# Performance work log

Hardware: AMD Instinct MI355X
Metric: run time of the kernel (lower is better)

## Reference

```python
import jax, jax.numpy as jnp
import numpy as np

N_ATOMS = 16384
B_GRAPHS = 64
K_CLUSTERS = 64          # clusters per molecule
M_CLUSTERS = B_GRAPHS * K_CLUSTERS
HID = 256                # hidden_channels (== node_attr feature dim)
FIL = 256                # num_filters
ECH = 64                 # edge_channels (num gaussians)
L_INT = 6                # num_interactions
CUTOFF = 10.0
LN2 = float(np.log(2.0))


def _ssp(x):
    # ShiftedSoftplus
    return jax.nn.softplus(x) - LN2


def setup_inputs() -> dict:
    key = jax.random.key(0)
    ks = jax.random.split(key, 12)
    pos = jax.random.normal(ks[0], (N_ATOMS, 3), jnp.float32) * 2.0
    node_attr = jax.random.normal(ks[1], (N_ATOMS, HID), jnp.float32)
    atoms_per_cluster = N_ATOMS // M_CLUSTERS
    subgraph_index = (jnp.arange(N_ATOMS) // atoms_per_cluster).astype(jnp.int64)
    batch = (jnp.arange(N_ATOMS) // (N_ATOMS // B_GRAPHS)).astype(jnp.int64)
    s = 0.05
    params = {
        "mlp_w1": jax.random.normal(ks[2], (L_INT, ECH, FIL), jnp.float32) * s,
        "mlp_b1": jnp.zeros((L_INT, FIL), jnp.float32),
        "mlp_w2": jax.random.normal(ks[3], (L_INT, FIL, FIL), jnp.float32) * s,
        "mlp_b2": jnp.zeros((L_INT, FIL), jnp.float32),
        "lin1_w": jax.random.normal(ks[4], (L_INT, HID, FIL), jnp.float32) * s,  # no bias
        "lin2_w": jax.random.normal(ks[5], (L_INT, FIL, HID), jnp.float32) * s,
        "lin2_b": jnp.zeros((L_INT, HID), jnp.float32),
        "lin_w":  jax.random.normal(ks[6], (L_INT, HID, HID), jnp.float32) * s,
        "lin_b":  jnp.zeros((L_INT, HID), jnp.float32),
    }
    return {"pos": pos, "node_attr": node_attr,
            "subgraph_index": subgraph_index, "batch": batch,
            "num_graphs": B_GRAPHS, "clusters_per_graph": K_CLUSTERS, **params}


def _complete_graph_edges(num_graphs, clusters_per_graph):
    # static (numpy) construction of per-molecule complete graph, no self loops
    K = clusters_per_graph
    i = np.arange(K)
    pr, pc = np.meshgrid(i, i, indexing='ij')
    m = pr != pc
    pr, pc = pr[m], pc[m]                       # (K*(K-1),)
    off = np.arange(num_graphs)[:, None] * K    # (B,1)
    row = jnp.asarray((off + pr[None, :]).reshape(-1))
    col = jnp.asarray((off + pc[None, :]).reshape(-1))
    return row, col


def reference(pos, node_attr, subgraph_index, batch, num_graphs, clusters_per_graph,
              mlp_w1, mlp_b1, mlp_w2, mlp_b2, lin1_w, lin2_w, lin2_b, lin_w, lin_b):
    M = num_graphs * clusters_per_graph
    # ---- coarse_grain: scatter-mean atoms into clusters ----
    cnt = jax.ops.segment_sum(jnp.ones((pos.shape[0],), pos.dtype), subgraph_index, num_segments=M)
    cnt = jnp.maximum(cnt, 1.0)[:, None]
    cluster_pos = jax.ops.segment_sum(pos, subgraph_index, num_segments=M) / cnt        # (M,3)
    cluster_attr = jax.ops.segment_sum(node_attr, subgraph_index, num_segments=M) / cnt  # (M,H)

    # ---- complete graph per molecule ----
    row, col = _complete_graph_edges(num_graphs, clusters_per_graph)
    edge_length = jnp.linalg.norm(cluster_pos[row] - cluster_pos[col], axis=1)          # (E,)

    # ---- GaussianSmearing ----
    offset = jnp.linspace(0.0, CUTOFF, ECH)
    coeff = -0.5 / (offset[1] - offset[0]) ** 2
    edge_attr = jnp.exp(coeff * (edge_length[:, None] - offset[None, :]) ** 2)          # (E,ECH)

    # smooth cutoff envelope
    C = 0.5 * (jnp.cos(edge_length * jnp.pi / CUTOFF) + 1.0)
    C = C * (edge_length <= CUTOFF).astype(C.dtype)                                     # (E,)

    # ---- SchNetEncoder (embed_node=False) ----
    h = cluster_attr
    for l in range(L_INT):
        # filter-generating MLP
        W = _ssp(edge_attr @ mlp_w1[l] + mlp_b1[l]) @ mlp_w2[l] + mlp_b2[l]             # (E,F)
        W = W * C[:, None]
        x = h @ lin1_w[l]                                                               # (M,F)
        agg = jax.ops.segment_sum(x[row] * W, col, num_segments=M)                      # (M,F)
        x = agg @ lin2_w[l] + lin2_b[l]                                                 # (M,H)
        x = _ssp(x)
        x = x @ lin_w[l] + lin_b[l]
        h = h + x                                                                       # residual
    return h
```

## Files before the change

### kernel.cpp

```cpp
#include <hip/hip_runtime.h>
#include <cstdint>

#define NATOMS 16384
#define BGRAPH 64
#define KC     64
#define MCL    (BGRAPH*KC)
#define HIDC   256
#define FILC   256
#define ECHC   64
#define LINT   6

#define TGRID  2048
#define NBP    2112

typedef __bf16 bf16x8 __attribute__((ext_vector_type(8)));
typedef __bf16 bf16x2 __attribute__((ext_vector_type(2)));
typedef float  f32x4  __attribute__((ext_vector_type(4)));
typedef unsigned short u16x8 __attribute__((ext_vector_type(8)));

__device__ __forceinline__ float bf2f(unsigned short u) {
    unsigned int x = ((unsigned int)u) << 16;
    return __builtin_bit_cast(float, x);
}
__device__ __forceinline__ unsigned short f2bf(float f) {
    __bf16 h = (__bf16)f;
    return __builtin_bit_cast(unsigned short, h);
}
__device__ __forceinline__ unsigned int pk2(float a, float b) {
    bf16x2 v = { (__bf16)a, (__bf16)b };
    return __builtin_bit_cast(unsigned int, v);
}
__device__ __forceinline__ float ssp_poly(float x) {
    float u = fminf(x * x, 4.0f);
    float q = u * fmaf(u, fmaf(u, 3.4722222e-4f, -5.2083333e-3f), 0.125f);
    return fmaf(0.5f, x, q);
}
__device__ __forceinline__ float ssp_fast(float x) {
    float m = fmaxf(x, 0.0f);
    float t = __builtin_amdgcn_exp2f(-fabsf(x) * 1.44269504088896341f);
    float l = __builtin_amdgcn_logf(1.0f + t);
    return fmaf(0.69314718055994531f, l, m - 0.69314718055994531f);
}
__device__ __forceinline__ int sw_off(int row, int col) {
    int s = (row + (row >> 3)) & 7;
    return row * 256 + ((((col >> 3) ^ s) << 3) | (col & 7));
}
__device__ __forceinline__ int phi_sw(int row) {
    return ((row & 7) ^ ((row >> 3) & 7)) & 7;
}

#define CGB   1024
#define N_W1  (LINT*16384)
#define N_BIG (LINT*65536)
#define PACK_BLOCKS ((N_W1 + 4*N_BIG + 255)/256)
__global__ void k_prep(const float* __restrict__ pos, const float* __restrict__ attr,
                       const int* __restrict__ subi,
                       float* __restrict__ h, unsigned short* __restrict__ h_bf,
                       float* __restrict__ cpos,
                       const float* __restrict__ w1_src, const float* __restrict__ w2_src,
                       const float* __restrict__ l1_src, const float* __restrict__ l2_src,
                       const float* __restrict__ lw_src,
                       unsigned short* __restrict__ w1p, unsigned short* __restrict__ w2p,
                       unsigned short* __restrict__ l1p, unsigned short* __restrict__ l2p,
                       unsigned short* __restrict__ lwp)
{
    if (blockIdx.x >= CGB) {
        int idx = (blockIdx.x - CGB) * 256 + threadIdx.x;
        if (idx < N_W1) {
            int j = idx & 7, lane = (idx >> 3) & 63, kt = (idx >> 9) & 1;
            int mt = (idx >> 10) & 15, l = idx >> 14;
            int ech = kt*32 + (lane >> 4)*8 + j;
            int f1  = mt*16 + (lane & 15);
            w1p[idx] = f2bf(w1_src[(l*64 + ech)*256 + f1]);
            return;
        }
        int r = idx - N_W1;
        int which = r / N_BIG;
        if (which >= 4) return;
        int e = r - which * N_BIG;
        const float* src = (which == 0) ? w2_src : (which == 1) ? l1_src
                         : (which == 2) ? l2_src : lw_src;
        unsigned short* dst = (which == 0) ? w2p : (which == 1) ? l1p
                            : (which == 2) ? l2p : lwp;
        int n = e % 256;
        int k = (e / 256) % 256;
        int l = e / 65536;
        int nt = n >> 4, kt = k >> 5, q = (k >> 3) & 3, j = k & 7;
        int lane = q*16 + (n & 15);
        dst[l*65536 + ((nt*8 + kt)*64 + lane)*8 + j] = f2bf(src[e]);
        return;
    }
    const int m = blockIdx.x * 4 + (threadIdx.x >> 6);
    const int lane = threadIdx.x & 63;
    const bool is64 = (subi[8] == 1);
    int lo = 0, hi = NATOMS;
    while (lo < hi) { int mid = (lo + hi) >> 1;
        int v = is64 ? subi[2*mid] : subi[mid];
        if (v < m) lo = mid + 1; else hi = mid; }
    int lo2 = lo, hi2 = NATOMS;
    while (lo2 < hi2) { int mid = (lo2 + hi2) >> 1;
        int v = is64 ? subi[2*mid] : subi[mid];
        if (v < m + 1) lo2 = mid + 1; else hi2 = mid; }
    const int cnt2 = lo2 - lo;
    const float inv = 1.0f / (float)(cnt2 > 0 ? cnt2 : 1);

    float4 s = {0.f, 0.f, 0.f, 0.f};
    for (int a = lo; a < lo2; a++) {
        const float4 v = *reinterpret_cast<const float4*>(&attr[a*HIDC + lane*4]);
        s.x += v.x; s.y += v.y; s.z += v.z; s.w += v.w;
    }
    s.x *= inv; s.y *= inv; s.z *= inv; s.w *= inv;
    *reinterpret_cast<float4*>(&h[m*HIDC + lane*4]) = s;
    const int o = m*HIDC + lane*4;
    h_bf[o+0] = f2bf(s.x); h_bf[o+1] = f2bf(s.y);
    h_bf[o+2] = f2bf(s.z); h_bf[o+3] = f2bf(s.w);
    if (lane < 3) {
        float p = 0.f;
        for (int a = lo; a < lo2; a++) p += pos[a*3 + lane];
        cpos[m*3 + lane] = p * inv;
    }
}

__device__ __forceinline__ void gemm16x2(const unsigned short* A_s, const unsigned short* Bp,
                                         int w, int lane, f32x4 acc[2])
{
    const int quad = lane >> 4, l16 = lane & 15;
    const int s = (l16 + (l16 >> 3)) & 7;
    acc[0] = f32x4{0.f,0.f,0.f,0.f};
    acc[1] = f32x4{0.f,0.f,0.f,0.f};
    #pragma unroll
    for (int kt = 0; kt < 8; kt++) {
        bf16x8 afr = *reinterpret_cast<const bf16x8*>(&A_s[l16*256 + (((kt*4 + quad) ^ s) << 3)]);
        #pragma unroll
        for (int nt = 0; nt < 2; nt++) {
            bf16x8 bfr = *reinterpret_cast<const bf16x8*>(Bp + (((w*2 + nt)*8 + kt)*64 + lane)*8);
            acc[nt] = __builtin_amdgcn_mfma_f32_16x16x32_bf16(afr, bfr, acc[nt], 0, 0, 0);
        }
    }
}

__device__ __forceinline__ void gemm16w16(const unsigned short* A_s, const unsigned short* Bp,
                                          int w, int lane, f32x4& acc)
{
    const int quad = lane >> 4, l16 = lane & 15;
    const int s = (l16 + (l16 >> 3)) & 7;
    acc = f32x4{0.f,0.f,0.f,0.f};
    #pragma unroll
    for (int kt = 0; kt < 8; kt++) {
        bf16x8 afr = *reinterpret_cast<const bf16x8*>(&A_s[l16*256 + (((kt*4 + quad) ^ s) << 3)]);
        bf16x8 bfr = *reinterpret_cast<const bf16x8*>(Bp + (((w*8 + kt)*64 + lane))*8);
        acc = __builtin_amdgcn_mfma_f32_16x16x32_bf16(afr, bfr, acc, 0, 0, 0);
    }
}

#define NTB   (LINT*33)
#define OSTR  264
__global__ __launch_bounds__(512) void k_tab(
    const unsigned short* __restrict__ w1p_all, const unsigned short* __restrict__ w2p_all,
    const float* __restrict__ b1_all, const float* __restrict__ b2_all,
    unsigned short* __restrict__ table,
    const unsigned short* __restrict__ h_bf, const unsigned short* __restrict__ lin1p,
    unsigned short* __restrict__ x0buf)
{
    __shared__ unsigned short G_s[64 * 256];
    __shared__ unsigned short phi_s[16 * OSTR];
    __shared__ float C_s[64];
    __shared__ float d_s[64];

    const int t  = threadIdx.x;
    const int w  = t >> 6, lane = t & 63;
    const int quad = lane >> 4, l16 = lane & 15;

    if (blockIdx.x >= NTB) {
        const int mb = blockIdx.x - NTB;
        unsigned short* A_s = G_s;
        {
            int r = t >> 5, seg = t & 31;
            int s = (r + (r >> 3)) & 7;
            u16x8 v = *reinterpret_cast<const u16x8*>(h_bf + (size_t)(mb*16 + r)*256 + seg*8);
            *reinterpret_cast<u16x8*>(&A_s[r*256 + ((seg ^ s) << 3)]) = v;
        }
        __syncthreads();
        f32x4 acc[2];
        gemm16x2(A_s, lin1p, w, lane, acc);
        #pragma unroll
        for (int nt = 0; nt < 2; nt++) {
            int col = (w*2 + nt)*16 + l16;
            #pragma unroll
            for (int i = 0; i < 4; i++)
                x0buf[(size_t)(mb*16 + quad*4 + i)*256 + col] = f2bf(acc[nt][i]);
        }
        return;
    }

    const int l  = blockIdx.x / 33;
    const int g0 = (blockIdx.x % 33) * 64;
    const unsigned short* w1p = w1p_all + (size_t)l*16384;
    const unsigned short* w2p = w2p_all + (size_t)l*65536;
    const float* b1 = b1_all + l*256;
    const float* b2 = b2_all + l*256;

    if (t < 64) {
        float d = (float)(g0 + t) * 0.0048828125f;
        d_s[t] = d;
        float Cv = 0.5f * (__cosf(d * 0.31415926535897932f) + 1.0f);
        C_s[t] = (d <= 10.0f) ? Cv : 0.0f;
    }
    __syncthreads();

    const float DELTA = 10.0f / 63.0f;
    const float C2 = (-0.5f / (DELTA * DELTA)) * 1.44269504088896341f;
    {
        float d = d_s[lane];
        u16x8 ph;
        #pragma unroll
        for (int j = 0; j < 8; j++) {
            float diff = d - (float)(w*8 + j) * DELTA;
            ph[j] = f2bf(__builtin_amdgcn_exp2f(C2 * diff * diff));
        }
        *reinterpret_cast<u16x8*>(&phi_s[lane*64 + ((w ^ phi_sw(lane)) << 3)]) = ph;
    }
    __syncthreads();

    f32x4 acc1[2][4];
    #pragma unroll
    for (int mt = 0; mt < 2; mt++) {
        const int f1b = (w*2 + mt)*16 + quad*4;
        float4 bq = *reinterpret_cast<const float4*>(&b1[f1b]);
        #pragma unroll
        for (int nt = 0; nt < 4; nt++) {
            acc1[mt][nt][0] = bq.x; acc1[mt][nt][1] = bq.y;
            acc1[mt][nt][2] = bq.z; acc1[mt][nt][3] = bq.w;
        }
    }
    #pragma unroll
    for (int kt = 0; kt < 2; kt++) {
        bf16x8 bfr[4];
        #pragma unroll
        for (int nt = 0; nt < 4; nt++) {
            int row = nt*16 + l16;
            bfr[nt] = *reinterpret_cast<const bf16x8*>(
                &phi_s[row*64 + (((kt*4 + quad) ^ phi_sw(row)) << 3)]);
        }
        #pragma unroll
        for (int mt = 0; mt < 2; mt++) {
            bf16x8 afr = *reinterpret_cast<const bf16x8*>(
                w1p + (((w*2 + mt)*2 + kt)*64 + lane)*8);
            #pragma unroll
            for (int nt = 0; nt < 4; nt++)
                acc1[mt][nt] = __builtin_amdgcn_mfma_f32_16x16x32_bf16(afr, bfr[nt], acc1[mt][nt], 0, 0, 0);
        }
    }

    float Cn[4];
    #pragma unroll
    for (int nt = 0; nt < 4; nt++) Cn[nt] = C_s[nt*16 + l16];

    #pragma unroll
    for (int mt = 0; mt < 2; mt++) {
        const int f1b = (w*2 + mt)*16 + quad*4;
        #pragma unroll
        for (int nt = 0; nt < 4; nt++) {
            float v0 = ssp_poly(acc1[mt][nt][0]) * Cn[nt];
            float v1 = ssp_poly(acc1[mt][nt][1]) * Cn[nt];
            float v2 = ssp_poly(acc1[mt][nt][2]) * Cn[nt];
            float v3 = ssp_poly(acc1[mt][nt][3]) * Cn[nt];
            uint2 pp;
            pp.x = pk2(v0, v1);
            pp.y = pk2(v2, v3);
            int edge = nt*16 + l16;
            int s = (edge + (edge >> 3)) & 7;
            int a = edge*256 + ((((f1b >> 3) ^ s) << 3) | (f1b & 7));
            *reinterpret_cast<uint2*>(&G_s[a]) = pp;
        }
    }
    __syncthreads();

    f32x4 acc2[4][2];
    #pragma unroll
    for (int a = 0; a < 4; a++)
        #pragma unroll
        for (int bb = 0; bb < 2; bb++) acc2[a][bb] = f32x4{0.f,0.f,0.f,0.f};

    #pragma unroll
    for (int kt = 0; kt < 8; kt++) {
        bf16x8 afr[4];
        #pragma unroll
        for (int mt = 0; mt < 4; mt++) {
            int row = mt*16 + l16;
            int s = (row + (row >> 3)) & 7;
            afr[mt] = *reinterpret_cast<const bf16x8*>(&G_s[row*256 + (((kt*4 + quad) ^ s) << 3)]);
        }
        #pragma unroll
        for (int nt = 0; nt < 2; nt++) {
            const int ntg = w*2 + nt;
            bf16x8 bfr = *reinterpret_cast<const bf16x8*>(w2p + ((ntg*8 + kt)*64 + lane)*8);
            #pragma unroll
            for (int mt = 0; mt < 4; mt++)
                acc2[mt][nt] = __builtin_amdgcn_mfma_f32_16x16x32_bf16(afr[mt], bfr, acc2[mt][nt], 0, 0, 0);
        }
    }

    unsigned short* base = table + (size_t)l*NBP*256;
    #pragma unroll
    for (int nt = 0; nt < 2; nt++) {
        const int f = (w*2 + nt)*16 + l16;
        const float b2v = b2[f];
        #pragma unroll
        for (int mt = 0; mt < 4; mt++) {
            #pragma unroll
            for (int i = 0; i < 4; i++) {
                int e = mt*16 + quad*4 + i;
                base[(size_t)(g0 + e)*256 + f] =
                    f2bf(fmaf(C_s[e], b2v, acc2[mt][nt][i]));
            }
        }
    }
}

template<int DO_X>
__global__ __launch_bounds__(1024) void k_layer(
    const float* __restrict__ cpos,
    const unsigned short* __restrict__ xin, unsigned short* __restrict__ xout,
    const unsigned short* __restrict__ Tp,
    const unsigned short* __restrict__ lin2p, const float* __restrict__ lin2_b,
    const unsigned short* __restrict__ linp,  const float* __restrict__ lin_b,
    const unsigned short* __restrict__ lin1p,
    float* __restrict__ h)
{
    __shared__ unsigned short x_s[64 * 256];
    __shared__ unsigned short A0[16 * 256];
    __shared__ unsigned short A1[16 * 256];
    __shared__ int idx_s[1024];

    const int blk = blockIdx.x;
    const int b = blk >> 2, q = blk & 3;
    const int t = threadIdx.x;
    const int w = t >> 6, lane = t & 63, quad = lane >> 4, l16 = lane & 15;

    {
        int r = t >> 4, seg = t & 15;
        const u16x8* s8 = reinterpret_cast<const u16x8*>(
            xin + ((size_t)(b*64 + r))*256 + seg*16);
        u16x8* dst = reinterpret_cast<u16x8*>(&x_s[r*256 + seg*16]);
        dst[0] = s8[0]; dst[1] = s8[1];
    }
    {
        int r = t >> 4, cc = t & 15;
        int gr = b*64 + r, gc = b*64 + q*16 + cc;
        float ax = cpos[gr*3 + 0] - cpos[gc*3 + 0];
        float ay = cpos[gr*3 + 1] - cpos[gc*3 + 1];
        float az = cpos[gr*3 + 2] - cpos[gc*3 + 2];
        float d = sqrtf(ax*ax + ay*ay + az*az);
        int i;
        if (gr == gc || d >= 10.0f) i = TGRID;
        else {
            i = (int)fmaf(d, 204.8f, 0.5f);
            if (i > TGRID) i = TGRID;
        }
        idx_s[t] = i * 256;
    }
    __syncthreads();

    {
        const int c   = t >> 6;
        const int fc2 = t & 63;
        float a4[4] = {0.f, 0.f, 0.f, 0.f};
        #pragma unroll 8
        for (int r = 0; r < 64; r++) {
            const int pi = __builtin_amdgcn_readfirstlane(idx_s[r*16 + c]);
            const ushort4 t4 = *reinterpret_cast<const ushort4*>(Tp + pi + fc2*4);
            const ushort4 x4 = *reinterpret_cast<const ushort4*>(&x_s[r*256 + fc2*4]);
            a4[0] = fmaf(bf2f(x4.x), bf2f(t4.x), a4[0]);
            a4[1] = fmaf(bf2f(x4.y), bf2f(t4.y), a4[1]);
            a4[2] = fmaf(bf2f(x4.z), bf2f(t4.z), a4[2]);
            a4[3] = fmaf(bf2f(x4.w), bf2f(t4.w), a4[3]);
        }
        uint2 pv;
        pv.x = pk2(a4[0], a4[1]);
        pv.y = pk2(a4[2], a4[3]);
        int s2 = (c + (c >> 3)) & 7;
        *reinterpret_cast<uint2*>(
            &A0[c*256 + ((((fc2 >> 1) ^ s2) << 3) | ((fc2 & 1) * 4))]) = pv;
    }
    __syncthreads();

    const int col = w*16 + l16;
    const int rbase_g = b*64 + q*16;
    f32x4 acc;
    gemm16w16(A0, lin2p, w, lane, acc);
    float bv = lin2_b[col];
    #pragma unroll
    for (int i = 0; i < 4; i++)
        A1[sw_off(quad*4 + i, col)] = f2bf(ssp_fast(acc[i] + bv));
    __syncthreads();

    gemm16w16(A1, linp, w, lane, acc);
    bv = lin_b[col];
    float hv[4];
    #pragma unroll
    for (int i = 0; i < 4; i++) {
        int rg = rbase_g + quad*4 + i;
        float v = acc[i] + bv + h[(size_t)rg*256 + col];
        h[(size_t)rg*256 + col] = v;
        hv[i] = v;
    }
    if (DO_X) {
        #pragma unroll
        for (int i = 0; i < 4; i++)
            A0[sw_off(quad*4 + i, col)] = f2bf(hv[i]);
        __syncthreads();
        gemm16w16(A0, lin1p, w, lane, acc);
        #pragma unroll
        for (int i = 0; i < 4; i++) {
            int rg = rbase_g + quad*4 + i;
            xout[(size_t)rg*256 + col] = f2bf(acc[i]);
        }
    }
}

extern "C" void kernel_launch(void* const* d_in, const int* in_sizes, int n_in,
                              void* d_out, int out_size, void* d_ws, size_t ws_size,
                              hipStream_t stream)
{
    const float* pos    = (const float*)d_in[0];
    const float* nattr  = (const float*)d_in[1];
    const int*   subi   = (const int*)d_in[2];
    const float* mlp_w1 = (const float*)d_in[6];
    const float* mlp_b1 = (const float*)d_in[7];
    const float* mlp_w2 = (const float*)d_in[8];
    const float* mlp_b2 = (const float*)d_in[9];
    const float* lin1_w = (const float*)d_in[10];
    const float* lin2_w = (const float*)d_in[11];
    const float* lin2_b = (const float*)d_in[12];
    const float* lin_w  = (const float*)d_in[13];
    const float* lin_b  = (const float*)d_in[14];
    float* h = (float*)d_out;

    char* p = (char*)d_ws;
    auto alloc = [&](size_t bytes) { char* r = p; p += (bytes + 255) & ~(size_t)255; return r; };
    unsigned short* h_bf   = (unsigned short*)alloc((size_t)MCL*256*2);
    unsigned short* x0buf  = (unsigned short*)alloc((size_t)MCL*256*2);
    unsigned short* x1buf  = (unsigned short*)alloc((size_t)MCL*256*2);
    unsigned short* table  = (unsigned short*)alloc((size_t)LINT*NBP*256*2);
    float*          cpos   = (float*)alloc((size_t)MCL*3*4);
    unsigned short* w1p    = (unsigned short*)alloc((size_t)LINT*16384*2);
    unsigned short* w2p    = (unsigned short*)alloc((size_t)LINT*65536*2);
    unsigned short* lin1p  = (unsigned short*)alloc((size_t)LINT*65536*2);
    unsigned short* lin2p  = (unsigned short*)alloc((size_t)LINT*65536*2);
    unsigned short* linp   = (unsigned short*)alloc((size_t)LINT*65536*2);

    k_prep<<<CGB + PACK_BLOCKS, 256, 0, stream>>>(
        pos, nattr, subi, h, h_bf, cpos,
        mlp_w1, mlp_w2, lin1_w, lin2_w, lin_w,
        w1p, w2p, lin1p, lin2p, linp);

    k_tab<<<NTB + 256, 512, 0, stream>>>(w1p, w2p, mlp_b1, mlp_b2, table,
                                         h_bf, lin1p, x0buf);

    for (int l = 0; l < LINT; l++) {
        const unsigned short* xin  = (l & 1) ? x1buf : x0buf;
        unsigned short*       xout = (l & 1) ? x0buf : x1buf;
        const unsigned short* Tl = table + (size_t)l*NBP*256;
        if (l < LINT-1) {
            k_layer<1><<<BGRAPH*4, 1024, 0, stream>>>(cpos, xin, xout, Tl,
                lin2p + (size_t)l*65536, lin2_b + l*256,
                linp + (size_t)l*65536, lin_b + l*256,
                lin1p + (size_t)(l+1)*65536, h);
        } else {
            k_layer<0><<<BGRAPH*4, 1024, 0, stream>>>(cpos, xin, xout, Tl,
                lin2p + (size_t)l*65536, lin2_b + l*256,
                linp + (size_t)l*65536, lin_b + l*256,
                lin1p, h);
        }
    }
}
```

Before: 213.7 us.

## Fuse six layer kernels into one cooperative persistent kernel with grid sync

The six per-layer kernel launches become a single cooperative kernel that loops over layers and uses grid.sync between them. The initial lin1 projection of the cluster features moves out of the table kernel and into the fused kernel's prologue. The index computation from cluster positions is done once and kept in shared memory across layers. This removes launch overhead and repeated setup, but adds grid-wide barrier costs and requires all 256 blocks of 1024 threads to be co-resident.

```diff
diff --git a/kernel.cpp b/kernel.cpp
--- a/kernel.cpp
+++ b/kernel.cpp
@@ -1,4 +1,5 @@
 #include <hip/hip_runtime.h>
+#include <hip/hip_cooperative_groups.h>
 #include <cstdint>
 
 #define NATOMS 16384
@@ -121,46 +122,12 @@
     }
 }
 
-__device__ __forceinline__ void gemm16x2(const unsigned short* A_s, const unsigned short* Bp,
-                                         int w, int lane, f32x4 acc[2])
-{
-    const int quad = lane >> 4, l16 = lane & 15;
-    const int s = (l16 + (l16 >> 3)) & 7;
-    acc[0] = f32x4{0.f,0.f,0.f,0.f};
-    acc[1] = f32x4{0.f,0.f,0.f,0.f};
-    #pragma unroll
-    for (int kt = 0; kt < 8; kt++) {
-        bf16x8 afr = *reinterpret_cast<const bf16x8*>(&A_s[l16*256 + (((kt*4 + quad) ^ s) << 3)]);
-        #pragma unroll
-        for (int nt = 0; nt < 2; nt++) {
-            bf16x8 bfr = *reinterpret_cast<const bf16x8*>(Bp + (((w*2 + nt)*8 + kt)*64 + lane)*8);
-            acc[nt] = __builtin_amdgcn_mfma_f32_16x16x32_bf16(afr, bfr, acc[nt], 0, 0, 0);
-        }
-    }
-}
-
-__device__ __forceinline__ void gemm16w16(const unsigned short* A_s, const unsigned short* Bp,
-                                          int w, int lane, f32x4& acc)
-{
-    const int quad = lane >> 4, l16 = lane & 15;
-    const int s = (l16 + (l16 >> 3)) & 7;
-    acc = f32x4{0.f,0.f,0.f,0.f};
-    #pragma unroll
-    for (int kt = 0; kt < 8; kt++) {
-        bf16x8 afr = *reinterpret_cast<const bf16x8*>(&A_s[l16*256 + (((kt*4 + quad) ^ s) << 3)]);
-        bf16x8 bfr = *reinterpret_cast<const bf16x8*>(Bp + (((w*8 + kt)*64 + lane))*8);
-        acc = __builtin_amdgcn_mfma_f32_16x16x32_bf16(afr, bfr, acc, 0, 0, 0);
-    }
-}
-
 #define NTB   (LINT*33)
 #define OSTR  264
 __global__ __launch_bounds__(512) void k_tab(
     const unsigned short* __restrict__ w1p_all, const unsigned short* __restrict__ w2p_all,
     const float* __restrict__ b1_all, const float* __restrict__ b2_all,
-    unsigned short* __restrict__ table,
-    const unsigned short* __restrict__ h_bf, const unsigned short* __restrict__ lin1p,
-    unsigned short* __restrict__ x0buf)
+    unsigned short* __restrict__ table)
 {
     __shared__ unsigned short G_s[64 * 256];
     __shared__ unsigned short phi_s[16 * OSTR];
@@ -170,28 +137,6 @@
     const int t  = threadIdx.x;
     const int w  = t >> 6, lane = t & 63;
     const int quad = lane >> 4, l16 = lane & 15;
-
-    if (blockIdx.x >= NTB) {
-        const int mb = blockIdx.x - NTB;
-        unsigned short* A_s = G_s;
-        {
-            int r = t >> 5, seg = t & 31;
-            int s = (r + (r >> 3)) & 7;
-            u16x8 v = *reinterpret_cast<const u16x8*>(h_bf + (size_t)(mb*16 + r)*256 + seg*8);
-            *reinterpret_cast<u16x8*>(&A_s[r*256 + ((seg ^ s) << 3)]) = v;
-        }
-        __syncthreads();
-        f32x4 acc[2];
-        gemm16x2(A_s, lin1p, w, lane, acc);
-        #pragma unroll
-        for (int nt = 0; nt < 2; nt++) {
-            int col = (w*2 + nt)*16 + l16;
-            #pragma unroll
-            for (int i = 0; i < 4; i++)
-                x0buf[(size_t)(mb*16 + quad*4 + i)*256 + col] = f2bf(acc[nt][i]);
-        }
-        return;
-    }
 
     const int l  = blockIdx.x / 33;
     const int g0 = (blockIdx.x % 33) * 64;
@@ -318,11 +263,24 @@
     }
 }
 
-template<int DO_X>
-__global__ __launch_bounds__(1024) void k_layer(
-    const float* __restrict__ cpos,
-    const unsigned short* __restrict__ xin, unsigned short* __restrict__ xout,
-    const unsigned short* __restrict__ Tp,
+__device__ __forceinline__ void gemm16w16(const unsigned short* A_s, const unsigned short* Bp,
+                                          int w, int lane, f32x4& acc)
+{
+    const int quad = lane >> 4, l16 = lane & 15;
+    const int s = (l16 + (l16 >> 3)) & 7;
+    acc = f32x4{0.f,0.f,0.f,0.f};
+    #pragma unroll
+    for (int kt = 0; kt < 8; kt++) {
+        bf16x8 afr = *reinterpret_cast<const bf16x8*>(&A_s[l16*256 + (((kt*4 + quad) ^ s) << 3)]);
+        bf16x8 bfr = *reinterpret_cast<const bf16x8*>(Bp + (((w*8 + kt)*64 + lane))*8);
+        acc = __builtin_amdgcn_mfma_f32_16x16x32_bf16(afr, bfr, acc, 0, 0, 0);
+    }
+}
+
+__global__ __launch_bounds__(1024) void k_layers(
+    const float* __restrict__ cpos, const unsigned short* __restrict__ h_bf,
+    unsigned short* __restrict__ xbuf0, unsigned short* __restrict__ xbuf1,
+    const unsigned short* __restrict__ table,
     const unsigned short* __restrict__ lin2p, const float* __restrict__ lin2_b,
     const unsigned short* __restrict__ linp,  const float* __restrict__ lin_b,
     const unsigned short* __restrict__ lin1p,
@@ -333,21 +291,17 @@
     __shared__ unsigned short A1[16 * 256];
     __shared__ int idx_s[1024];
 
+    cooperative_groups::grid_group grid = cooperative_groups::this_grid();
+
     const int blk = blockIdx.x;
     const int b = blk >> 2, q = blk & 3;
     const int t = threadIdx.x;
     const int w = t >> 6, lane = t & 63, quad = lane >> 4, l16 = lane & 15;
-
-    {
-        int r = t >> 4, seg = t & 15;
-        const u16x8* s8 = reinterpret_cast<const u16x8*>(
-            xin + ((size_t)(b*64 + r))*256 + seg*16);
-        u16x8* dst = reinterpret_cast<u16x8*>(&x_s[r*256 + seg*16]);
-        dst[0] = s8[0]; dst[1] = s8[1];
-    }
+    const int rbase_g = b*64 + q*16;
+
     {
         int r = t >> 4, cc = t & 15;
-        int gr = b*64 + r, gc = b*64 + q*16 + cc;
+        int gr = b*64 + r, gc = rbase_g + cc;
         float ax = cpos[gr*3 + 0] - cpos[gc*3 + 0];
         float ay = cpos[gr*3 + 1] - cpos[gc*3 + 1];
         float az = cpos[gr*3 + 2] - cpos[gc*3 + 2];
@@ -360,61 +314,112 @@
         }
         idx_s[t] = i * 256;
     }
+    {
+        int r = t >> 4, seg = t & 15;
+        int s = (r + (r >> 3)) & 7;
+        const u16x8* src = reinterpret_cast<const u16x8*>(
+            h_bf + (size_t)(b*64 + r)*256 + seg*16);
+        int c = seg*2;
+        *reinterpret_cast<u16x8*>(&x_s[r*256 + (((c  ) ^ s) << 3)]) = src[0];
+        *reinterpret_cast<u16x8*>(&x_s[r*256 + (((c+1) ^ s) << 3)]) = src[1];
+    }
     __syncthreads();
-
     {
-        const int c   = t >> 6;
-        const int fc2 = t & 63;
-        float a4[4] = {0.f, 0.f, 0.f, 0.f};
-        #pragma unroll 8
-        for (int r = 0; r < 64; r++) {
-            const int pi = __builtin_amdgcn_readfirstlane(idx_s[r*16 + c]);
-            const ushort4 t4 = *reinterpret_cast<const ushort4*>(Tp + pi + fc2*4);
-            const ushort4 x4 = *reinterpret_cast<const ushort4*>(&x_s[r*256 + fc2*4]);
-            a4[0] = fmaf(bf2f(x4.x), bf2f(t4.x), a4[0]);
-            a4[1] = fmaf(bf2f(x4.y), bf2f(t4.y), a4[1]);
-            a4[2] = fmaf(bf2f(x4.z), bf2f(t4.z), a4[2]);
-            a4[3] = fmaf(bf2f(x4.w), bf2f(t4.w), a4[3]);
-        }
-        uint2 pv;
-        pv.x = pk2(a4[0], a4[1]);
-        pv.y = pk2(a4[2], a4[3]);
-        int s2 = (c + (c >> 3)) & 7;
-        *reinterpret_cast<uint2*>(
-            &A0[c*256 + ((((fc2 >> 1) ^ s2) << 3) | ((fc2 & 1) * 4))]) = pv;
+        const int mt = w & 3, nb = w >> 2;
+        const int arow = mt*16 + l16;
+        const int s = (arow + (arow >> 3)) & 7;
+        f32x4 a4[4];
+        #pragma unroll
+        for (int nt = 0; nt < 4; nt++) a4[nt] = f32x4{0.f,0.f,0.f,0.f};
+        #pragma unroll
+        for (int kt = 0; kt < 8; kt++) {
+            bf16x8 afr = *reinterpret_cast<const bf16x8*>(
+                &x_s[arow*256 + (((kt*4 + quad) ^ s) << 3)]);
+            #pragma unroll
+            for (int nt = 0; nt < 4; nt++) {
+                bf16x8 bfr = *reinterpret_cast<const bf16x8*>(
+                    lin1p + (((nb*4 + nt)*8 + kt)*64 + lane)*8);
+                a4[nt] = __builtin_amdgcn_mfma_f32_16x16x32_bf16(afr, bfr, a4[nt], 0, 0, 0);
+            }
+        }
+        __syncthreads();
+        #pragma unroll
+        for (int nt = 0; nt < 4; nt++) {
+            int col = (nb*4 + nt)*16 + l16;
+            #pragma unroll
+            for (int i = 0; i < 4; i++)
+                x_s[(mt*16 + quad*4 + i)*256 + col] = f2bf(a4[nt][i]);
+        }
     }
     __syncthreads();
 
-    const int col = w*16 + l16;
-    const int rbase_g = b*64 + q*16;
-    f32x4 acc;
-    gemm16w16(A0, lin2p, w, lane, acc);
-    float bv = lin2_b[col];
-    #pragma unroll
-    for (int i = 0; i < 4; i++)
-        A1[sw_off(quad*4 + i, col)] = f2bf(ssp_fast(acc[i] + bv));
-    __syncthreads();
-
-    gemm16w16(A1, linp, w, lane, acc);
-    bv = lin_b[col];
-    float hv[4];
-    #pragma unroll
-    for (int i = 0; i < 4; i++) {
-        int rg = rbase_g + quad*4 + i;
-        float v = acc[i] + bv + h[(size_t)rg*256 + col];
-        h[(size_t)rg*256 + col] = v;
-        hv[i] = v;
-    }
-    if (DO_X) {
+    for (int l = 0; l < LINT; l++) {
+        if (l > 0) {
+            const unsigned short* xin = ((l-1) & 1) ? xbuf1 : xbuf0;
+            int r = t >> 4, seg = t & 15;
+            const u16x8* s8 = reinterpret_cast<const u16x8*>(
+                xin + ((size_t)(b*64 + r))*256 + seg*16);
+            u16x8* dst = reinterpret_cast<u16x8*>(&x_s[r*256 + seg*16]);
+            dst[0] = s8[0]; dst[1] = s8[1];
+            __syncthreads();
+        }
+        const unsigned short* Tl = table + (size_t)l*NBP*256;
+
+        {
+            const int c   = t >> 6;
+            const int fc2 = t & 63;
+            float a4[4] = {0.f, 0.f, 0.f, 0.f};
+            #pragma unroll 8
+            for (int r = 0; r < 64; r++) {
+                const int pi = __builtin_amdgcn_readfirstlane(idx_s[r*16 + c]);
+                const ushort4 t4 = *reinterpret_cast<const ushort4*>(Tl + pi + fc2*4);
+                const ushort4 x4 = *reinterpret_cast<const ushort4*>(&x_s[r*256 + fc2*4]);
+                a4[0] = fmaf(bf2f(x4.x), bf2f(t4.x), a4[0]);
+                a4[1] = fmaf(bf2f(x4.y), bf2f(t4.y), a4[1]);
+                a4[2] = fmaf(bf2f(x4.z), bf2f(t4.z), a4[2]);
+                a4[3] = fmaf(bf2f(x4.w), bf2f(t4.w), a4[3]);
+            }
+            uint2 pv;
+            pv.x = pk2(a4[0], a4[1]);
+            pv.y = pk2(a4[2], a4[3]);
+            int s2 = (c + (c >> 3)) & 7;
+            *reinterpret_cast<uint2*>(
+                &A0[c*256 + ((((fc2 >> 1) ^ s2) << 3) | ((fc2 & 1) * 4))]) = pv;
+        }
+        __syncthreads();
+
+        const int col = w*16 + l16;
+        f32x4 acc;
+        gemm16w16(A0, lin2p + (size_t)l*65536, w, lane, acc);
+        float bv = lin2_b[l*256 + col];
         #pragma unroll
         for (int i = 0; i < 4; i++)
-            A0[sw_off(quad*4 + i, col)] = f2bf(hv[i]);
+            A1[sw_off(quad*4 + i, col)] = f2bf(ssp_fast(acc[i] + bv));
         __syncthreads();
-        gemm16w16(A0, lin1p, w, lane, acc);
+
+        gemm16w16(A1, linp + (size_t)l*65536, w, lane, acc);
+        bv = lin_b[l*256 + col];
+        float hv[4];
         #pragma unroll
         for (int i = 0; i < 4; i++) {
             int rg = rbase_g + quad*4 + i;
-            xout[(size_t)rg*256 + col] = f2bf(acc[i]);
+            float v = acc[i] + bv + h[(size_t)rg*256 + col];
+            h[(size_t)rg*256 + col] = v;
+            hv[i] = v;
+        }
+        if (l < LINT-1) {
+            #pragma unroll
+            for (int i = 0; i < 4; i++)
+                A0[sw_off(quad*4 + i, col)] = f2bf(hv[i]);
+            __syncthreads();
+            gemm16w16(A0, lin1p + (size_t)(l+1)*65536, w, lane, acc);
+            unsigned short* xout = (l & 1) ? xbuf1 : xbuf0;
+            #pragma unroll
+            for (int i = 0; i < 4; i++) {
+                int rg = rbase_g + quad*4 + i;
+                xout[(size_t)rg*256 + col] = f2bf(acc[i]);
+            }
+            grid.sync();
         }
     }
 }
@@ -455,23 +460,11 @@
         mlp_w1, mlp_w2, lin1_w, lin2_w, lin_w,
         w1p, w2p, lin1p, lin2p, linp);
 
-    k_tab<<<NTB + 256, 512, 0, stream>>>(w1p, w2p, mlp_b1, mlp_b2, table,
-                                         h_bf, lin1p, x0buf);
-
-    for (int l = 0; l < LINT; l++) {
-        const unsigned short* xin  = (l & 1) ? x1buf : x0buf;
-        unsigned short*       xout = (l & 1) ? x0buf : x1buf;
-        const unsigned short* Tl = table + (size_t)l*NBP*256;
-        if (l < LINT-1) {
-            k_layer<1><<<BGRAPH*4, 1024, 0, stream>>>(cpos, xin, xout, Tl,
-                lin2p + (size_t)l*65536, lin2_b + l*256,
-                linp + (size_t)l*65536, lin_b + l*256,
-                lin1p + (size_t)(l+1)*65536, h);
-        } else {
-            k_layer<0><<<BGRAPH*4, 1024, 0, stream>>>(cpos, xin, xout, Tl,
-                lin2p + (size_t)l*65536, lin2_b + l*256,
-                linp + (size_t)l*65536, lin_b + l*256,
-                lin1p, h);
-        }
-    }
-}
+    k_tab<<<NTB, 512, 0, stream>>>(w1p, w2p, mlp_b1, mlp_b2, table);
+
+    void* args[] = { (void*)&cpos, (void*)&h_bf, (void*)&x0buf, (void*)&x1buf,
+                     (void*)&table, (void*)&lin2p, (void*)&lin2_b, (void*)&linp,
+                     (void*)&lin_b, (void*)&lin1p, (void*)&h };
+    hipLaunchCooperativeKernel((const void*)k_layers, dim3(BGRAPH*4), dim3(1024),
+                               args, 0, stream);
+}
```

Result: slower. 430.3 us (+101.3%).
